# Optimization experiments

Measured on AMD Instinct MI355X. Metric: run time of the kernel, lower is better.

The kernel has to match this reference:

```python
import jax, jax.numpy as jnp
import numpy as np

N_OR = 8          # orientations of the SE(2) discretization
BN_EPS = 1e-5


def _rotate_kernel(W, theta):
    """Rotate a spatial kernel [..., k, k] about its center by theta.
    Bilinear interpolation, zeros outside the kernel support."""
    k = W.shape[-1]
    c = (k - 1) / 2.0
    ys, xs = jnp.meshgrid(jnp.arange(k, dtype=jnp.float32) - c,
                          jnp.arange(k, dtype=jnp.float32) - c, indexing="ij")
    cos, sin = jnp.cos(theta), jnp.sin(theta)
    sy = cos * ys - sin * xs + c   # source coords: rotate sample grid by -theta
    sx = sin * ys + cos * xs + c
    y0 = jnp.floor(sy).astype(jnp.int32)
    x0 = jnp.floor(sx).astype(jnp.int32)
    wy = (sy - y0).astype(W.dtype)
    wx = (sx - x0).astype(W.dtype)

    def gather(yi, xi):
        valid = ((yi >= 0) & (yi < k) & (xi >= 0) & (xi < k)).astype(W.dtype)
        yc = jnp.clip(yi, 0, k - 1)
        xc = jnp.clip(xi, 0, k - 1)
        return W[..., yc, xc] * valid

    return (gather(y0, x0) * (1 - wy) * (1 - wx)
            + gather(y0, x0 + 1) * (1 - wy) * wx
            + gather(y0 + 1, x0) * wy * (1 - wx)
            + gather(y0 + 1, x0 + 1) * wy * wx)


def _thetas():
    return 2.0 * jnp.pi * jnp.arange(N_OR, dtype=jnp.float32) / N_OR


def _lift(x, W):
    """LiftM2Cartesian. x: [B,Cin,H,W] (pre-padded), W: [Cout,Cin,k,k].
    Returns [B,Cout,8,H',W']."""
    Wr = jax.vmap(lambda t: _rotate_kernel(W, t))(_thetas())  # [8,Cout,Cin,k,k]
    co = W.shape[0]
    Wf = Wr.reshape((N_OR * co,) + W.shape[1:])
    y = jax.lax.conv_general_dilated(x, Wf, (1, 1), "VALID",
                                     dimension_numbers=("NCHW", "OIHW", "NCHW"))
    B, _, H, Wd = y.shape
    return y.reshape(B, N_OR, co, H, Wd).transpose(0, 2, 1, 3, 4)


def _gconv(x, K):
    """ConvM2Cartesian. x: [B,Cin,8,H,W] (spatially pre-padded),
    K: [Cout,Cin,8,k,k]. Output orientation m uses the kernel spatially
    rotated by theta_m with the orientation axis cyclically shifted by m."""
    cout, cin, _, k, _ = K.shape
    # orient_idx[m, o] = (o - m) mod 8
    orient_idx = (jnp.arange(N_OR)[None, :] - jnp.arange(N_OR)[:, None]) % N_OR
    Kshift = jnp.moveaxis(K[:, :, orient_idx], 2, 0)        # [8m,Cout,Cin,8o,k,k]
    Km = jax.vmap(_rotate_kernel)(Kshift, _thetas())         # [8m,Cout,Cin,8o,k,k]
    Kf = Km.reshape(N_OR * cout, cin * N_OR, k, k)
    B, _, _, H, Wd = x.shape
    xf = x.reshape(B, cin * N_OR, H, Wd)
    y = jax.lax.conv_general_dilated(xf, Kf, (1, 1), "VALID",
                                     dimension_numbers=("NCHW", "OIHW", "NCHW"))
    Ho, Wo = y.shape[-2:]
    return y.reshape(B, N_OR, cout, Ho, Wo).transpose(0, 2, 1, 3, 4)


def _bn3d(x, gamma, beta):
    """BatchNorm3d (training-mode batch statistics). x: [B,C,O,H,W]."""
    mean = jnp.mean(x, axis=(0, 2, 3, 4), keepdims=True)
    var = jnp.mean((x - mean) ** 2, axis=(0, 2, 3, 4), keepdims=True)
    g = gamma.reshape(1, -1, 1, 1, 1)
    b = beta.reshape(1, -1, 1, 1, 1)
    return g * (x - mean) * jax.lax.rsqrt(var + BN_EPS) + b


def _pad_m2(x, p):
    return jnp.pad(x, ((0, 0), (0, 0), (0, 0), (p, p), (p, p)), mode="reflect")


def setup_inputs() -> dict:
    key = jax.random.key(0)
    ks = jax.random.split(key, 8)
    c = 16
    cin = 3
    x = jax.random.normal(ks[0], (2, cin, 256, 256), dtype=jnp.float32)
    lift_w = jax.random.normal(ks[1], (c, cin, 7, 7), dtype=jnp.float32) / np.sqrt(cin * 49)
    w1 = jax.random.normal(ks[2], (c, c, N_OR, 5, 5), dtype=jnp.float32) / np.sqrt(c * N_OR * 25)
    w2 = jax.random.normal(ks[3], (c, c, N_OR, 5, 5), dtype=jnp.float32) / np.sqrt(c * N_OR * 25)
    w3 = jax.random.normal(ks[4], (c, c, N_OR, 5, 5), dtype=jnp.float32) / np.sqrt(c * N_OR * 25)
    w4 = jax.random.normal(ks[5], (c, c, N_OR, 1, 1), dtype=jnp.float32) / np.sqrt(c * N_OR)
    final_w = jax.random.normal(ks[6], (1, c), dtype=jnp.float32) / np.sqrt(c)
    ones = jnp.ones((c,), dtype=jnp.float32)
    zeros = jnp.zeros((c,), dtype=jnp.float32)
    return {"x": x, "lift_w": lift_w, "w1": w1, "w2": w2, "w3": w3, "w4": w4,
            "final_w": final_w,
            "g0": ones, "b0": zeros, "g1": ones, "b1": zeros, "g2": ones,
            "b2": zeros, "g3": ones, "b3": zeros, "g4": ones, "b4": zeros}


def reference(x, lift_w, w1, w2, w3, w4, final_w,
              g0, b0, g1, b1, g2, b2, g3, b3, g4, b4):
    # lift: ReflectionPad2d(3) -> LiftM2Cartesian(7) -> BN3d -> ReLU
    xp = jnp.pad(x, ((0, 0), (0, 0), (3, 3), (3, 3)), mode="reflect")
    h = jax.nn.relu(_bn3d(_lift(xp, lift_w), g0, b0))          # [B,16,8,H,W]
    # conv1..3: ReflectionPadM2(2) -> ConvM2Cartesian(5) -> BN3d -> ReLU (Dropout3d is identity in eval)
    h = jax.nn.relu(_bn3d(_gconv(_pad_m2(h, 2), w1), g1, b1))
    h = jax.nn.relu(_bn3d(_gconv(_pad_m2(h, 2), w2), g2, b2))
    h = jax.nn.relu(_bn3d(_gconv(_pad_m2(h, 2), w3), g3, b3))
    # conv4: 1x1 group conv -> BN3d -> ReLU
    h = jax.nn.relu(_bn3d(_gconv(h, w4), g4, b4))
    # MaxProjectM2: max over orientation axis
    h = jnp.max(h, axis=2)                                     # [B,16,H,W]
    # final 1x1 conv (no bias) + sigmoid
    return jax.nn.sigmoid(jnp.einsum("bchw,oc->bohw", h, final_w))
```

## Files before the change

kernel.cpp:

```cpp
#include <hip/hip_runtime.h>
#include <hip/hip_bf16.h>
#include <math.h>

#define HW 65536
#define WID 256
#define NOR 8
#define PLANE_C (NOR * HW)
#define PLANE_B (16 * NOR * HW)
#define BN_N 1048576.0f
#define NHWC_STRIDE 136

typedef __attribute__((ext_vector_type(8)))  short  short8;
typedef __attribute__((ext_vector_type(4)))  short  short4v;
typedef __attribute__((ext_vector_type(16))) float  float16;
typedef __attribute__((ext_vector_type(4)))  float  float4v;

__device__ __forceinline__ float b2f(short s) {
    union { unsigned int u; float f; } c;
    c.u = ((unsigned int)(unsigned short)s) << 16;
    return c.f;
}
__device__ __forceinline__ short f2b(float f) {
    union { __hip_bfloat16 h; short s; } c;
    c.h = __float2bfloat16(f);
    return c.s;
}

__global__ void detect_k(const void* __restrict__ x, int* __restrict__ flag) {
    __shared__ int bad;
    if (threadIdx.x == 0) bad = 0;
    __syncthreads();
    const __hip_bfloat16* p = (const __hip_bfloat16*)x;
    for (int i = threadIdx.x; i < 4096; i += 256) {
        float v = __bfloat162float(p[i]);
        if (!(fabsf(v) < 1e4f)) atomicOr(&bad, 1);
    }
    __syncthreads();
    if (threadIdx.x == 0) *flag = bad ? 0 : 1;
}

#define CVT_TOTAL 551392
__global__ void cvt_all_k(const void* p0, const void* p1, const void* p2, const void* p3,
                          const void* p4, const void* p5, const void* p6, const void* p7,
                          const void* p8, const void* p9, const void* p10, const void* p11,
                          const void* p12, const void* p13, const void* p14, const void* p15,
                          const void* p16, float* __restrict__ dst, const int* __restrict__ flag) {
    int i = blockIdx.x * 512 + threadIdx.x;
    if (i >= CVT_TOTAL) return;
    const void* src; int off;
    if      (i < 393216) { src = p0;  off = 0; }
    else if (i < 395568) { src = p1;  off = 393216; }
    else if (i < 446768) { src = p2;  off = 395568; }
    else if (i < 497968) { src = p3;  off = 446768; }
    else if (i < 549168) { src = p4;  off = 497968; }
    else if (i < 551216) { src = p5;  off = 549168; }
    else if (i < 551232) { src = p6;  off = 551216; }
    else if (i < 551248) { src = p7;  off = 551232; }
    else if (i < 551264) { src = p8;  off = 551248; }
    else if (i < 551280) { src = p9;  off = 551264; }
    else if (i < 551296) { src = p10; off = 551280; }
    else if (i < 551312) { src = p11; off = 551296; }
    else if (i < 551328) { src = p12; off = 551312; }
    else if (i < 551344) { src = p13; off = 551328; }
    else if (i < 551360) { src = p14; off = 551344; }
    else if (i < 551376) { src = p15; off = 551360; }
    else                 { src = p16; off = 551376; }
    int j = i - off;
    dst[i] = (*flag) ? __bfloat162float(((const __hip_bfloat16*)src)[j])
                     : ((const float*)src)[j];
}

__device__ float rot_sample(const float* __restrict__ W, int k, float theta, int i, int j) {
    float c = 0.5f * (float)(k - 1);
    float ys = (float)i - c, xs = (float)j - c;
    float cs = cosf(theta), sn = sinf(theta);
    float sy = cs * ys - sn * xs + c;
    float sx = sn * ys + cs * xs + c;
    float fy = floorf(sy), fx = floorf(sx);
    int y0 = (int)fy, x0 = (int)fx;
    float wy = sy - fy, wx = sx - fx;
    float v00 = (y0 >= 0 && y0 < k && x0 >= 0 && x0 < k)                 ? W[y0 * k + x0]           : 0.f;
    float v01 = (y0 >= 0 && y0 < k && x0 + 1 >= 0 && x0 + 1 < k)         ? W[y0 * k + x0 + 1]       : 0.f;
    float v10 = (y0 + 1 >= 0 && y0 + 1 < k && x0 >= 0 && x0 < k)         ? W[(y0 + 1) * k + x0]     : 0.f;
    float v11 = (y0 + 1 >= 0 && y0 + 1 < k && x0 + 1 >= 0 && x0 + 1 < k) ? W[(y0 + 1) * k + x0 + 1] : 0.f;
    return v00 * (1 - wy) * (1 - wx) + v01 * (1 - wy) * wx
         + v10 * wy * (1 - wx) + v11 * wy * wx;
}

__device__ __forceinline__ float theta_of(int m) {
    return (6.2831855f * (float)m) / 8.0f;
}

__device__ __forceinline__ int mirror(int i) {
    i = i < 0 ? -i : i;
    return i >= WID ? (2 * WID - 2 - i) : i;
}

#define PK_BLIFT 20480
#define PK_BG 409600
#define PK_TOTAL (PK_BLIFT + 3 * PK_BG + 16384)
__global__ void mega_pack_k(const float* __restrict__ lwF, const float* __restrict__ w1F,
                            const float* __restrict__ w2F, const float* __restrict__ w3F,
                            const float* __restrict__ w4F,
                            __hip_bfloat16* __restrict__ Blift, __hip_bfloat16* __restrict__ Bg1,
                            __hip_bfloat16* __restrict__ Bg2, __hip_bfloat16* __restrict__ Bg3,
                            __hip_bfloat16* __restrict__ B1, float* __restrict__ statsL) {
    int idx = blockIdx.x * 256 + threadIdx.x;
    if (idx < 160) statsL[idx] = 0.f;
    if (idx >= PK_TOTAL) return;
    if (idx < PK_BLIFT) {
        int n = idx / 160, k = idx % 160;
        float v = 0.f;
        if (k < 147) {
            int c = n >> 3, o = n & 7;
            int ci = k / 49, s = k % 49;
            v = rot_sample(lwF + (c * 3 + ci) * 49, 7, theta_of(o), s / 7, s % 7);
        }
        Blift[idx] = __float2bfloat16(v);
        return;
    }
    idx -= PK_BLIFT;
    if (idx < 3 * PK_BG) {
        int l = idx / PK_BG;
        int r = idx - l * PK_BG;
        const float* w = (l == 0) ? w1F : ((l == 1) ? w2F : w3F);
        __hip_bfloat16* Bg = (l == 0) ? Bg1 : ((l == 1) ? Bg2 : Bg3);
        int j = r & 7;
        int n = (r >> 3) & 127;
        int kc4 = (r >> 10) & 3;
        int sq = r >> 12;
        int s = sq % 25, q = sq / 25;
        int ch = q * 32 + kc4 * 8 + j;
        int co = n >> 3, m = n & 7, ci = ch >> 3, o = ch & 7;
        int oo = (o - m + 8) & 7;
        Bg[r] = __float2bfloat16(
            rot_sample(w + ((co * 16 + ci) * 8 + oo) * 25, 5, theta_of(m), s / 5, s % 5));
        return;
    }
    idx -= 3 * PK_BG;
    {
        int n = idx >> 7, ch = idx & 127;
        int co = n >> 3, m = n & 7, ci = ch >> 3, o = ch & 7;
        B1[idx] = __float2bfloat16(w4F[(co * 16 + ci) * 8 + ((o - m + 8) & 7)]);
    }
}

__device__ __forceinline__ void stats_reduce8(const float16* acc, int lane, int l31,
                                              float* sred) {
#pragma unroll
    for (int nt = 0; nt < 4; nt++) {
        float sv = 0.f, s2v = 0.f;
#pragma unroll
        for (int g = 0; g < 2; g++)
#pragma unroll
            for (int r = 0; r < 16; r++) {
                float v = acc[g * 4 + nt][r];
                sv += v;
                s2v += v * v;
            }
#pragma unroll
        for (int off = 1; off <= 4; off <<= 1) {
            sv += __shfl_xor(sv, off);
            s2v += __shfl_xor(s2v, off);
        }
        sv += __shfl_xor(sv, 32);
        s2v += __shfl_xor(s2v, 32);
        if ((lane & 39) == 0) {
            int c = nt * 4 + (l31 >> 3);
            atomicAdd(&sred[c], sv);
            atomicAdd(&sred[16 + c], s2v);
        }
    }
}

__global__ __launch_bounds__(256, 2) void lift_fused_k(const float* __restrict__ xF,
                                                       const __hip_bfloat16* __restrict__ Bh,
                                                       __hip_bfloat16* __restrict__ nh_out,
                                                       float* __restrict__ stats) {
    __shared__ float Xs[3 * 484];
    __shared__ short tb[32768];
    __shared__ float sred[32];
    const short* B = (const short*)Bh;
    int tid = threadIdx.x;
    if (tid < 32) sred[tid] = 0.f;
    int tile = blockIdx.x;
    int b = blockIdx.y;
    int tx0 = (tile & 15) << 4, ty0 = (tile >> 4) << 4;
    for (int i = tid; i < 1452; i += 256) {
        int ci = i / 484, p = i - ci * 484;
        int yl = p / 22, xl = p - yl * 22;
        int gy = mirror(ty0 - 3 + yl), gx = mirror(tx0 - 3 + xl);
        Xs[i] = xF[((size_t)b * 3 + ci) * HW + gy * WID + gx];
    }
    __syncthreads();
    int wave = tid >> 6, lane = tid & 63;
    int l31 = lane & 31, half = lane >> 5;
    float16 acc[8];
#pragma unroll
    for (int i = 0; i < 8; i++) acc[i] = (float16)0.f;
    int pxl0 = wave * 64 + l31;
    int py0 = pxl0 >> 4, px0 = pxl0 & 15;
    int py1 = (pxl0 + 32) >> 4, px1 = (pxl0 + 32) & 15;
    const short* bp = B + (size_t)l31 * 160 + half * 8;
#pragma unroll
    for (int ks = 0; ks < 10; ks++) {
        short8 a0, a1;
#pragma unroll
        for (int j = 0; j < 8; j++) {
            int k = ks * 16 + half * 8 + j;
            float v0 = 0.f, v1 = 0.f;
            if (k < 147) {
                int ci = (k < 49) ? 0 : ((k < 98) ? 1 : 2);
                int s = k - ci * 49;
                int sy = s / 7, sx = s - sy * 7;
                v0 = Xs[ci * 484 + (py0 + sy) * 22 + px0 + sx];
                v1 = Xs[ci * 484 + (py1 + sy) * 22 + px1 + sx];
            }
            a0[j] = f2b(v0);
            a1[j] = f2b(v1);
        }
#pragma unroll
        for (int nt = 0; nt < 4; nt++) {
            short8 bb = *(const short8*)(bp + nt * 32 * 160 + ks * 16);
            acc[nt]     = __builtin_amdgcn_mfma_f32_32x32x16_bf16(a0, bb, acc[nt], 0, 0, 0);
            acc[4 + nt] = __builtin_amdgcn_mfma_f32_32x32x16_bf16(a1, bb, acc[4 + nt], 0, 0, 0);
        }
    }
#pragma unroll
    for (int g = 0; g < 2; g++)
#pragma unroll
        for (int nt = 0; nt < 4; nt++) {
            int ch = nt * 32 + l31;
#pragma unroll
            for (int r4 = 0; r4 < 4; r4++) {
                int pxb = wave * 64 + g * 32 + 8 * r4 + 4 * half;
#pragma unroll
                for (int i = 0; i < 4; i++)
                    tb[(pxb + i) * 128 + ch] = f2b(acc[g * 4 + nt][r4 * 4 + i]);
            }
        }
    __syncthreads();
    short* outp = (short*)nh_out + (size_t)b * HW * NHWC_STRIDE;
    for (int i = tid; i < 4096; i += 256) {
        int pxl = i >> 4, seg = i & 15;
        int y = ty0 + (pxl >> 4), x = tx0 + (pxl & 15);
        *(short8*)(outp + ((size_t)y * WID + x) * NHWC_STRIDE + seg * 8) =
            *(const short8*)&tb[pxl * 128 + seg * 8];
    }
    stats_reduce8(acc, lane, l31, sred);
    __syncthreads();
    if (tid < 16) {
        atomicAdd(&stats[tid * 2], sred[tid]);
        atomicAdd(&stats[tid * 2 + 1], sred[16 + tid]);
    }
}

__global__ __launch_bounds__(256, 2) void gconv_mfma_k(const __hip_bfloat16* __restrict__ nh_in,
                                                       const __hip_bfloat16* __restrict__ Bgh,
                                                       __hip_bfloat16* __restrict__ nh_out,
                                                       const float* __restrict__ statsPrev,
                                                       const float* __restrict__ gPrev,
                                                       const float* __restrict__ bPrev,
                                                       float* __restrict__ statsNew) {
    __shared__ short Au[32768];
    __shared__ float ssl[32];
    __shared__ float sred[32];
    const short* nhwc = (const short*)nh_in;
    const short* Bg = (const short*)Bgh;
    int bid = blockIdx.x;
    int xcd = bid & 7, qt = bid >> 3;
    int b = xcd >> 2, band = xcd & 3;
    int tx0 = (qt & 15) << 4;
    int ty0 = (band << 6) + ((qt >> 4) << 4);
    int tid = threadIdx.x;
    if (tid < 32) sred[tid] = 0.f;
    if (tid < 16) {
        float mean = statsPrev[tid * 2] / BN_N;
        float var = statsPrev[tid * 2 + 1] / BN_N - mean * mean;
        float sc = gPrev[tid] * rsqrtf(var + 1e-5f);
        ssl[tid * 2] = sc;
        ssl[tid * 2 + 1] = bPrev[tid] - mean * sc;
    }
    int w = tid >> 6, lane = tid & 63;
    int pxg = w & 1, nhf = w >> 1;
    int l15 = lane & 15, l4 = lane >> 4;
    float4v acc[32];
#pragma unroll
    for (int i = 0; i < 32; i++) acc[i] = (float4v)0.f;
    const size_t bbase = (size_t)b * HW;
    const int nb = nhf << 6;

    for (int h = 0; h < 2; h++) {
        __syncthreads();
        for (int i = tid; i < 3200; i += 256) {
            int kc = i / 400, p = i - kc * 400;
            int yl = p / 20, xl = p - yl * 20;
            int gy = mirror(ty0 - 2 + yl);
            int gx = mirror(tx0 - 2 + xl);
            short8 raw = *(const short8*)(nhwc + (bbase + gy * WID + gx) * NHWC_STRIDE
                                          + h * 64 + kc * 8);
            int c = h * 8 + kc;
            float sc = ssl[c * 2], sh = ssl[c * 2 + 1];
            short8 ov;
#pragma unroll
            for (int e = 0; e < 8; e++)
                ov[e] = f2b(fmaxf(fmaf(b2f(raw[e]), sc, sh), 0.f));
            *(short8*)&Au[(kc * 441 + yl * 21 + xl) * 8] = ov;
        }
        __syncthreads();
        for (int s = 0; s < 25; s++) {
            int dy = s / 5 - 2, dx = s % 5 - 2;
#pragma unroll
            for (int kq = 0; kq < 2; kq++) {
                int abase = (kq * 4 + l4) * 441 + ((pxg << 3) + 2 + dy) * 21 + (l15 + 2 + dx);
                const short* brow = Bg
                    + ((size_t)(((((h * 2 + kq) * 25 + s) << 2) + l4)) * 128 + nb + l15) * 8;
                short8 a[8];
#pragma unroll
                for (int r = 0; r < 8; r++)
                    a[r] = *(const short8*)&Au[(abase + r * 21) * 8];
#pragma unroll
                for (int nt = 0; nt < 4; nt++) {
                    short8 bb = *(const short8*)(brow + nt * 128);
#pragma unroll
                    for (int r = 0; r < 8; r++)
                        acc[r * 4 + nt] = __builtin_amdgcn_mfma_f32_16x16x32_bf16(
                            a[r], bb, acc[r * 4 + nt], 0, 0, 0);
                }
            }
        }
    }

    __syncthreads();
#pragma unroll
    for (int r = 0; r < 8; r++) {
        int pxl = ((pxg << 3) + r) * 16 + (l4 << 2);
#pragma unroll
        for (int nt = 0; nt < 4; nt++) {
            int n = nb + nt * 16 + l15;
#pragma unroll
            for (int e = 0; e < 4; e++)
                Au[(pxl + e) * 128 + n] = f2b(acc[r * 4 + nt][e]);
        }
    }
    __syncthreads();
    short* outp = (short*)nh_out;
    for (int i = tid; i < 4096; i += 256) {
        int pxl = i >> 4, seg = i & 15;
        int y = ty0 + (pxl >> 4), x = tx0 + (pxl & 15);
        *(short8*)(outp + (bbase + y * WID + x) * NHWC_STRIDE + seg * 8) =
            *(const short8*)&Au[pxl * 128 + seg * 8];
    }
#pragma unroll
    for (int nt = 0; nt < 4; nt++) {
        float sv = 0.f, s2v = 0.f;
#pragma unroll
        for (int r = 0; r < 8; r++)
#pragma unroll
            for (int e = 0; e < 4; e++) {
                float v = acc[r * 4 + nt][e];
                sv += v;
                s2v += v * v;
            }
#pragma unroll
        for (int off = 1; off <= 4; off <<= 1) {
            sv += __shfl_xor(sv, off);
            s2v += __shfl_xor(s2v, off);
        }
        sv += __shfl_xor(sv, 16);
        s2v += __shfl_xor(s2v, 16);
        sv += __shfl_xor(sv, 32);
        s2v += __shfl_xor(s2v, 32);
        if ((lane & 7) == 0 && l4 == 0) {
            int c = (nhf << 3) + (nt << 1) + (l15 >> 3);
            atomicAdd(&sred[c], sv);
            atomicAdd(&sred[16 + c], s2v);
        }
    }
    __syncthreads();
    if (tid < 16) {
        atomicAdd(&statsNew[tid * 2], sred[tid]);
        atomicAdd(&statsNew[tid * 2 + 1], sred[16 + tid]);
    }
}

__global__ __launch_bounds__(256, 2) void conv1x1_gemm_k(const __hip_bfloat16* __restrict__ nh,
                                                         const __hip_bfloat16* __restrict__ B1h,
                                                         __hip_bfloat16* __restrict__ outP,
                                                         const float* __restrict__ statsPrev,
                                                         const float* __restrict__ gPrev,
                                                         const float* __restrict__ bPrev,
                                                         float* __restrict__ statsNew) {
    __shared__ float sred[32];
    __shared__ float ssl[32];
    const short* nhwc = (const short*)nh;
    const short* B1 = (const short*)B1h;
    int tid = threadIdx.x;
    if (tid < 32) sred[tid] = 0.f;
    if (tid < 16) {
        float mean = statsPrev[tid * 2] / BN_N;
        float var = statsPrev[tid * 2 + 1] / BN_N - mean * mean;
        float sc = gPrev[tid] * rsqrtf(var + 1e-5f);
        ssl[tid * 2] = sc;
        ssl[tid * 2 + 1] = bPrev[tid] - mean * sc;
    }
    __syncthreads();
    int b = blockIdx.y;
    int wave = tid >> 6, lane = tid & 63;
    int l31 = lane & 31, half = lane >> 5;
    int p0 = blockIdx.x * 256 + wave * 64;
    float16 acc[8];
#pragma unroll
    for (int i = 0; i < 8; i++) acc[i] = (float16)0.f;
    const short* a0p = nhwc + ((size_t)b * HW + p0 + l31) * NHWC_STRIDE + half * 8;
    const short* a1p = a0p + 32 * NHWC_STRIDE;
    const short* bp  = B1 + (size_t)l31 * 128 + half * 8;
#pragma unroll
    for (int ks = 0; ks < 8; ks++) {
        short8 r0 = *(const short8*)(a0p + ks * 16);
        short8 r1 = *(const short8*)(a1p + ks * 16);
        int c = ks * 2 + half;
        float sc = ssl[c * 2], sh = ssl[c * 2 + 1];
        short8 a0, a1;
#pragma unroll
        for (int e = 0; e < 8; e++) {
            a0[e] = f2b(fmaxf(fmaf(b2f(r0[e]), sc, sh), 0.f));
            a1[e] = f2b(fmaxf(fmaf(b2f(r1[e]), sc, sh), 0.f));
        }
#pragma unroll
        for (int nt = 0; nt < 4; nt++) {
            short8 bb = *(const short8*)(bp + nt * 32 * 128 + ks * 16);
            acc[nt]     = __builtin_amdgcn_mfma_f32_32x32x16_bf16(a0, bb, acc[nt], 0, 0, 0);
            acc[4 + nt] = __builtin_amdgcn_mfma_f32_32x32x16_bf16(a1, bb, acc[4 + nt], 0, 0, 0);
        }
    }
    short* outb = (short*)outP + (size_t)b * PLANE_B;
#pragma unroll
    for (int g = 0; g < 2; g++)
#pragma unroll
        for (int nt = 0; nt < 4; nt++) {
            int n = nt * 32 + l31;
#pragma unroll
            for (int r4 = 0; r4 < 4; r4++) {
                int base = 8 * r4 + 4 * half;
                short4v v;
                v[0] = f2b(acc[g * 4 + nt][r4 * 4 + 0]);
                v[1] = f2b(acc[g * 4 + nt][r4 * 4 + 1]);
                v[2] = f2b(acc[g * 4 + nt][r4 * 4 + 2]);
                v[3] = f2b(acc[g * 4 + nt][r4 * 4 + 3]);
                *(short4v*)(outb + (size_t)n * HW + p0 + g * 32 + base) = v;
            }
        }
    stats_reduce8(acc, lane, l31, sred);
    __syncthreads();
    if (tid < 16) {
        atomicAdd(&statsNew[tid * 2], sred[tid]);
        atomicAdd(&statsNew[tid * 2 + 1], sred[16 + tid]);
    }
}

__global__ void final_k(const __hip_bfloat16* __restrict__ inP, const float* __restrict__ stats,
                        const float* __restrict__ g, const float* __restrict__ beta,
                        const float* __restrict__ fw, void* __restrict__ out,
                        const int* __restrict__ flag) {
    __shared__ float ssl[32];
    if (threadIdx.x < 16) {
        int c = threadIdx.x;
        float mean = stats[c * 2] / BN_N;
        float var = stats[c * 2 + 1] / BN_N - mean * mean;
        float sc = g[c] * rsqrtf(var + 1e-5f);
        ssl[c * 2] = sc;
        ssl[c * 2 + 1] = beta[c] - mean * sc;
    }
    __syncthreads();
    int i = blockIdx.x * blockDim.x + threadIdx.x;
    int b = i >> 16, pix = i & 65535;
    const short* inp = (const short*)inP;
    float acc = 0.f;
#pragma unroll
    for (int co = 0; co < 16; co++) {
        float sc = ssl[co * 2], sh = ssl[co * 2 + 1];
        float mx = 0.f;
        const short* p = inp + (size_t)b * PLANE_B + (size_t)co * PLANE_C + pix;
#pragma unroll
        for (int m = 0; m < 8; m++) mx = fmaxf(mx, fmaf(b2f(p[m * HW]), sc, sh));
        acc = fmaf(fw[co], mx, acc);
    }
    float r = 1.f / (1.f + expf(-acc));
    if (*flag)
        ((__hip_bfloat16*)out)[i] = __float2bfloat16(r);
    else
        ((float*)out)[i] = r;
}

extern "C" void kernel_launch(void* const* d_in, const int* in_sizes, int n_in,
                              void* d_out, int out_size, void* d_ws, size_t ws_size,
                              hipStream_t stream) {
    float* ws = (float*)d_ws;
    __hip_bfloat16* planarB = (__hip_bfloat16*)ws;
    __hip_bfloat16* nhwcA = (__hip_bfloat16*)(ws + 8388608);
    __hip_bfloat16* nhwcB = (__hip_bfloat16*)(ws + 17301504);
    __hip_bfloat16* Bg1   = (__hip_bfloat16*)(ws + 26214400);
    __hip_bfloat16* Bg2   = (__hip_bfloat16*)(ws + 26419200);
    __hip_bfloat16* Bg3   = (__hip_bfloat16*)(ws + 26624000);
    __hip_bfloat16* Blift = (__hip_bfloat16*)(ws + 26828800);
    __hip_bfloat16* B1    = (__hip_bfloat16*)(ws + 26839040);
    float* xF  = ws + 26847232;
    float* lwF = xF + 393216;
    float* w1F = lwF + 2352;
    float* w2F = w1F + 51200;
    float* w3F = w2F + 51200;
    float* w4F = w3F + 51200;
    float* fwF = w4F + 2048;
    float* gbF = fwF + 16;
    float* statsL = ws + 27398624;
    int*   flag   = (int*)(statsL + 160);

    detect_k<<<1, 256, 0, stream>>>(d_in[0], flag);
    cvt_all_k<<<(CVT_TOTAL + 511) / 512, 512, 0, stream>>>(
        d_in[0], d_in[1], d_in[2], d_in[3], d_in[4], d_in[5], d_in[6], d_in[7], d_in[8],
        d_in[9], d_in[10], d_in[11], d_in[12], d_in[13], d_in[14], d_in[15], d_in[16],
        xF, flag);

    mega_pack_k<<<(PK_TOTAL + 255) / 256, 256, 0, stream>>>(
        lwF, w1F, w2F, w3F, w4F, Blift, Bg1, Bg2, Bg3, B1, statsL);

    lift_fused_k<<<dim3(256, 2), 256, 0, stream>>>(xF, Blift, nhwcA, statsL);

    __hip_bfloat16* Bgs[3] = {Bg1, Bg2, Bg3};
    __hip_bfloat16* nio[4] = {nhwcA, nhwcB, nhwcA, nhwcB};
    for (int l = 0; l < 3; l++) {
        gconv_mfma_k<<<512, 256, 0, stream>>>(nio[l], Bgs[l], nio[l + 1],
                                              statsL + 32 * l, gbF + 32 * l, gbF + 32 * l + 16,
                                              statsL + 32 * (l + 1));
    }

    conv1x1_gemm_k<<<dim3(256, 2), 256, 0, stream>>>(nio[3], B1, planarB,
                                                     statsL + 96, gbF + 96, gbF + 112,
                                                     statsL + 128);

    final_k<<<(2 * HW) / 256, 256, 0, stream>>>(planarB, statsL + 128, gbF + 128, gbF + 144,
                                                fwF, d_out, flag);
}
```

Baseline: 458.1 us.

## Drop input conversion pass and reuse A-fragments across kernel rows in gconv

```diff
diff --git a/kernel.cpp b/kernel.cpp
--- a/kernel.cpp
+++ b/kernel.cpp
@@ -25,8 +25,16 @@
     c.h = __float2bfloat16(f);
     return c.s;
 }
-
-__global__ void detect_k(const void* __restrict__ x, int* __restrict__ flag) {
+__device__ __forceinline__ float ldv(const void* p, int i, int isbf) {
+    return isbf ? b2f(((const short*)p)[i]) : ((const float*)p)[i];
+}
+
+__global__ void detect_cvt_k(const void* x, const void* fw,
+                             const void* g0, const void* b0, const void* g1, const void* b1,
+                             const void* g2, const void* b2, const void* g3, const void* b3,
+                             const void* g4, const void* b4,
+                             float* __restrict__ gbF, float* __restrict__ fwF,
+                             int* __restrict__ flag) {
     __shared__ int bad;
     if (threadIdx.x == 0) bad = 0;
     __syncthreads();
@@ -36,41 +44,19 @@
         if (!(fabsf(v) < 1e4f)) atomicOr(&bad, 1);
     }
     __syncthreads();
-    if (threadIdx.x == 0) *flag = bad ? 0 : 1;
-}
-
-#define CVT_TOTAL 551392
-__global__ void cvt_all_k(const void* p0, const void* p1, const void* p2, const void* p3,
-                          const void* p4, const void* p5, const void* p6, const void* p7,
-                          const void* p8, const void* p9, const void* p10, const void* p11,
-                          const void* p12, const void* p13, const void* p14, const void* p15,
-                          const void* p16, float* __restrict__ dst, const int* __restrict__ flag) {
-    int i = blockIdx.x * 512 + threadIdx.x;
-    if (i >= CVT_TOTAL) return;
-    const void* src; int off;
-    if      (i < 393216) { src = p0;  off = 0; }
-    else if (i < 395568) { src = p1;  off = 393216; }
-    else if (i < 446768) { src = p2;  off = 395568; }
-    else if (i < 497968) { src = p3;  off = 446768; }
-    else if (i < 549168) { src = p4;  off = 497968; }
-    else if (i < 551216) { src = p5;  off = 549168; }
-    else if (i < 551232) { src = p6;  off = 551216; }
-    else if (i < 551248) { src = p7;  off = 551232; }
-    else if (i < 551264) { src = p8;  off = 551248; }
-    else if (i < 551280) { src = p9;  off = 551264; }
-    else if (i < 551296) { src = p10; off = 551280; }
-    else if (i < 551312) { src = p11; off = 551296; }
-    else if (i < 551328) { src = p12; off = 551312; }
-    else if (i < 551344) { src = p13; off = 551328; }
-    else if (i < 551360) { src = p14; off = 551344; }
-    else if (i < 551376) { src = p15; off = 551360; }
-    else                 { src = p16; off = 551376; }
-    int j = i - off;
-    dst[i] = (*flag) ? __bfloat162float(((const __hip_bfloat16*)src)[j])
-                     : ((const float*)src)[j];
-}
-
-__device__ float rot_sample(const float* __restrict__ W, int k, float theta, int i, int j) {
+    int isbf = bad ? 0 : 1;
+    if (threadIdx.x == 0) *flag = isbf;
+    int t = threadIdx.x;
+    if (t < 160) {
+        const void* srcs[10] = {g0, b0, g1, b1, g2, b2, g3, b3, g4, b4};
+        gbF[t] = ldv(srcs[t >> 4], t & 15, isbf);
+    } else if (t < 176) {
+        fwF[t - 160] = ldv(fw, t - 160, isbf);
+    }
+}
+
+__device__ float rot_sample_g(const void* __restrict__ W, int isbf, int k, float theta,
+                              int i, int j) {
     float c = 0.5f * (float)(k - 1);
     float ys = (float)i - c, xs = (float)j - c;
     float cs = cosf(theta), sn = sinf(theta);
@@ -79,10 +65,10 @@
     float fy = floorf(sy), fx = floorf(sx);
     int y0 = (int)fy, x0 = (int)fx;
     float wy = sy - fy, wx = sx - fx;
-    float v00 = (y0 >= 0 && y0 < k && x0 >= 0 && x0 < k)                 ? W[y0 * k + x0]           : 0.f;
-    float v01 = (y0 >= 0 && y0 < k && x0 + 1 >= 0 && x0 + 1 < k)         ? W[y0 * k + x0 + 1]       : 0.f;
-    float v10 = (y0 + 1 >= 0 && y0 + 1 < k && x0 >= 0 && x0 < k)         ? W[(y0 + 1) * k + x0]     : 0.f;
-    float v11 = (y0 + 1 >= 0 && y0 + 1 < k && x0 + 1 >= 0 && x0 + 1 < k) ? W[(y0 + 1) * k + x0 + 1] : 0.f;
+    float v00 = (y0 >= 0 && y0 < k && x0 >= 0 && x0 < k)                 ? ldv(W, y0 * k + x0, isbf)           : 0.f;
+    float v01 = (y0 >= 0 && y0 < k && x0 + 1 >= 0 && x0 + 1 < k)         ? ldv(W, y0 * k + x0 + 1, isbf)       : 0.f;
+    float v10 = (y0 + 1 >= 0 && y0 + 1 < k && x0 >= 0 && x0 < k)         ? ldv(W, (y0 + 1) * k + x0, isbf)     : 0.f;
+    float v11 = (y0 + 1 >= 0 && y0 + 1 < k && x0 + 1 >= 0 && x0 + 1 < k) ? ldv(W, (y0 + 1) * k + x0 + 1, isbf) : 0.f;
     return v00 * (1 - wy) * (1 - wx) + v01 * (1 - wy) * wx
          + v10 * wy * (1 - wx) + v11 * wy * wx;
 }
@@ -99,22 +85,27 @@
 #define PK_BLIFT 20480
 #define PK_BG 409600
 #define PK_TOTAL (PK_BLIFT + 3 * PK_BG + 16384)
-__global__ void mega_pack_k(const float* __restrict__ lwF, const float* __restrict__ w1F,
-                            const float* __restrict__ w2F, const float* __restrict__ w3F,
-                            const float* __restrict__ w4F,
+__global__ void mega_pack_k(const void* __restrict__ lw, const void* __restrict__ w1,
+                            const void* __restrict__ w2, const void* __restrict__ w3,
+                            const void* __restrict__ w4,
                             __hip_bfloat16* __restrict__ Blift, __hip_bfloat16* __restrict__ Bg1,
                             __hip_bfloat16* __restrict__ Bg2, __hip_bfloat16* __restrict__ Bg3,
-                            __hip_bfloat16* __restrict__ B1, float* __restrict__ statsL) {
+                            __hip_bfloat16* __restrict__ B1, float* __restrict__ statsL,
+                            const int* __restrict__ flag) {
     int idx = blockIdx.x * 256 + threadIdx.x;
     if (idx < 160) statsL[idx] = 0.f;
     if (idx >= PK_TOTAL) return;
+    int isbf = *flag;
     if (idx < PK_BLIFT) {
         int n = idx / 160, k = idx % 160;
         float v = 0.f;
         if (k < 147) {
             int c = n >> 3, o = n & 7;
             int ci = k / 49, s = k % 49;
-            v = rot_sample(lwF + (c * 3 + ci) * 49, 7, theta_of(o), s / 7, s % 7);
+            v = rot_sample_g((const char*)lw + 0, isbf, 7, theta_of(o), s / 7, s % 7);
+            v = rot_sample_g(isbf ? (const void*)((const short*)lw + (c * 3 + ci) * 49)
+                                  : (const void*)((const float*)lw + (c * 3 + ci) * 49),
+                             isbf, 7, theta_of(o), s / 7, s % 7);
         }
         Blift[idx] = __float2bfloat16(v);
         return;
@@ -123,7 +114,7 @@
     if (idx < 3 * PK_BG) {
         int l = idx / PK_BG;
         int r = idx - l * PK_BG;
-        const float* w = (l == 0) ? w1F : ((l == 1) ? w2F : w3F);
+        const void* w = (l == 0) ? w1 : ((l == 1) ? w2 : w3);
         __hip_bfloat16* Bg = (l == 0) ? Bg1 : ((l == 1) ? Bg2 : Bg3);
         int j = r & 7;
         int n = (r >> 3) & 127;
@@ -133,15 +124,17 @@
         int ch = q * 32 + kc4 * 8 + j;
         int co = n >> 3, m = n & 7, ci = ch >> 3, o = ch & 7;
         int oo = (o - m + 8) & 7;
-        Bg[r] = __float2bfloat16(
-            rot_sample(w + ((co * 16 + ci) * 8 + oo) * 25, 5, theta_of(m), s / 5, s % 5));
+        int off = ((co * 16 + ci) * 8 + oo) * 25;
+        const void* wp = isbf ? (const void*)((const short*)w + off)
+                              : (const void*)((const float*)w + off);
+        Bg[r] = __float2bfloat16(rot_sample_g(wp, isbf, 5, theta_of(m), s / 5, s % 5));
         return;
     }
     idx -= 3 * PK_BG;
     {
         int n = idx >> 7, ch = idx & 127;
         int co = n >> 3, m = n & 7, ci = ch >> 3, o = ch & 7;
-        B1[idx] = __float2bfloat16(w4F[(co * 16 + ci) * 8 + ((o - m + 8) & 7)]);
+        B1[idx] = __float2bfloat16(ldv(w4, (co * 16 + ci) * 8 + ((o - m + 8) & 7), isbf));
     }
 }
 
@@ -173,16 +166,18 @@
     }
 }
 
-__global__ __launch_bounds__(256, 2) void lift_fused_k(const float* __restrict__ xF,
+__global__ __launch_bounds__(256, 2) void lift_fused_k(const void* __restrict__ x,
                                                        const __hip_bfloat16* __restrict__ Bh,
                                                        __hip_bfloat16* __restrict__ nh_out,
-                                                       float* __restrict__ stats) {
+                                                       float* __restrict__ stats,
+                                                       const int* __restrict__ flag) {
     __shared__ float Xs[3 * 484];
     __shared__ short tb[32768];
     __shared__ float sred[32];
     const short* B = (const short*)Bh;
     int tid = threadIdx.x;
     if (tid < 32) sred[tid] = 0.f;
+    int isbf = *flag;
     int tile = blockIdx.x;
     int b = blockIdx.y;
     int tx0 = (tile & 15) << 4, ty0 = (tile >> 4) << 4;
@@ -190,7 +185,7 @@
         int ci = i / 484, p = i - ci * 484;
         int yl = p / 22, xl = p - yl * 22;
         int gy = mirror(ty0 - 3 + yl), gx = mirror(tx0 - 3 + xl);
-        Xs[i] = xF[((size_t)b * 3 + ci) * HW + gy * WID + gx];
+        Xs[i] = ldv(x, (int)(((size_t)b * 3 + ci) * HW) + gy * WID + gx, isbf);
     }
     __syncthreads();
     int wave = tid >> 6, lane = tid & 63;
@@ -243,8 +238,8 @@
     short* outp = (short*)nh_out + (size_t)b * HW * NHWC_STRIDE;
     for (int i = tid; i < 4096; i += 256) {
         int pxl = i >> 4, seg = i & 15;
-        int y = ty0 + (pxl >> 4), x = tx0 + (pxl & 15);
-        *(short8*)(outp + ((size_t)y * WID + x) * NHWC_STRIDE + seg * 8) =
+        int y = ty0 + (pxl >> 4), xx = tx0 + (pxl & 15);
+        *(short8*)(outp + ((size_t)y * WID + xx) * NHWC_STRIDE + seg * 8) =
             *(const short8*)&tb[pxl * 128 + seg * 8];
     }
     stats_reduce8(acc, lane, l31, sred);
@@ -308,24 +303,29 @@
             *(short8*)&Au[(kc * 441 + yl * 21 + xl) * 8] = ov;
         }
         __syncthreads();
-        for (int s = 0; s < 25; s++) {
-            int dy = s / 5 - 2, dx = s % 5 - 2;
-#pragma unroll
-            for (int kq = 0; kq < 2; kq++) {
-                int abase = (kq * 4 + l4) * 441 + ((pxg << 3) + 2 + dy) * 21 + (l15 + 2 + dx);
-                const short* brow = Bg
-                    + ((size_t)(((((h * 2 + kq) * 25 + s) << 2) + l4)) * 128 + nb + l15) * 8;
-                short8 a[8];
-#pragma unroll
-                for (int r = 0; r < 8; r++)
-                    a[r] = *(const short8*)&Au[(abase + r * 21) * 8];
-#pragma unroll
-                for (int nt = 0; nt < 4; nt++) {
-                    short8 bb = *(const short8*)(brow + nt * 128);
-#pragma unroll
-                    for (int r = 0; r < 8; r++)
-                        acc[r * 4 + nt] = __builtin_amdgcn_mfma_f32_16x16x32_bf16(
-                            a[r], bb, acc[r * 4 + nt], 0, 0, 0);
+#pragma unroll
+        for (int kq = 0; kq < 2; kq++) {
+            int kcol = (kq * 4 + l4) * 441;
+#pragma unroll
+            for (int dx0 = 0; dx0 < 5; dx0++) {
+                int base0 = kcol + (pxg << 3) * 21 + (l15 + dx0);
+                short8 a[12];
+#pragma unroll
+                for (int rr = 0; rr < 12; rr++)
+                    a[rr] = *(const short8*)&Au[(base0 + rr * 21) * 8];
+#pragma unroll
+                for (int dy0 = 0; dy0 < 5; dy0++) {
+                    int s = dy0 * 5 + dx0;
+                    const short* brow = Bg
+                        + ((size_t)(((((h * 2 + kq) * 25 + s) << 2) + l4)) * 128 + nb + l15) * 8;
+#pragma unroll
+                    for (int nt = 0; nt < 4; nt++) {
+                        short8 bb = *(const short8*)(brow + nt * 128);
+#pragma unroll
+                        for (int r = 0; r < 8; r++)
+                            acc[r * 4 + nt] = __builtin_amdgcn_mfma_f32_16x16x32_bf16(
+                                a[dy0 + r], bb, acc[r * 4 + nt], 0, 0, 0);
+                    }
                 }
             }
         }
@@ -505,27 +505,21 @@
     __hip_bfloat16* Bg3   = (__hip_bfloat16*)(ws + 26624000);
     __hip_bfloat16* Blift = (__hip_bfloat16*)(ws + 26828800);
     __hip_bfloat16* B1    = (__hip_bfloat16*)(ws + 26839040);
-    float* xF  = ws + 26847232;
-    float* lwF = xF + 393216;
-    float* w1F = lwF + 2352;
-    float* w2F = w1F + 51200;
-    float* w3F = w2F + 51200;
-    float* w4F = w3F + 51200;
-    float* fwF = w4F + 2048;
-    float* gbF = fwF + 16;
-    float* statsL = ws + 27398624;
+    float* gbF  = ws + 26847232;
+    float* fwF  = gbF + 160;
+    float* statsL = fwF + 16;
     int*   flag   = (int*)(statsL + 160);
 
-    detect_k<<<1, 256, 0, stream>>>(d_in[0], flag);
-    cvt_all_k<<<(CVT_TOTAL + 511) / 512, 512, 0, stream>>>(
-        d_in[0], d_in[1], d_in[2], d_in[3], d_in[4], d_in[5], d_in[6], d_in[7], d_in[8],
-        d_in[9], d_in[10], d_in[11], d_in[12], d_in[13], d_in[14], d_in[15], d_in[16],
-        xF, flag);
+    detect_cvt_k<<<1, 256, 0, stream>>>(d_in[0], d_in[6],
+                                        d_in[7], d_in[8], d_in[9], d_in[10], d_in[11],
+                                        d_in[12], d_in[13], d_in[14], d_in[15], d_in[16],
+                                        gbF, fwF, flag);
 
     mega_pack_k<<<(PK_TOTAL + 255) / 256, 256, 0, stream>>>(
-        lwF, w1F, w2F, w3F, w4F, Blift, Bg1, Bg2, Bg3, B1, statsL);
-
-    lift_fused_k<<<dim3(256, 2), 256, 0, stream>>>(xF, Blift, nhwcA, statsL);
+        d_in[1], d_in[2], d_in[3], d_in[4], d_in[5],
+        Blift, Bg1, Bg2, Bg3, B1, statsL, flag);
+
+    lift_fused_k<<<dim3(256, 2), 256, 0, stream>>>(d_in[0], Blift, nhwcA, statsL, flag);
 
     __hip_bfloat16* Bgs[3] = {Bg1, Bg2, Bg3};
     __hip_bfloat16* nio[4] = {nhwcA, nhwcB, nhwcA, nhwcB};
```

Result: no change. 455.7 us (-0.5%).
